# Kernel optimization log

Measured on AMD Instinct MI355X. Metric: run time of the kernel, lower is better.

Reference implementation:

```python
import jax, jax.numpy as jnp
import numpy as np

H = 1024      # hidden_dim
E = 512       # word_emb_dim
A = 512       # av_emb_dim
L = 512       # max_length
V = 50257     # n_vocab


def setup_inputs() -> dict:
    key = jax.random.key(0)
    ks = jax.random.split(key, 16)
    s = lambda k, shape, scale=0.02: (jax.random.normal(k, shape, dtype=jnp.float32) * scale)
    return {
        "word": jax.random.randint(ks[0], (1,), 0, V),
        "enc_seq_len": 1,
        "av_emb": s(ks[1], (1, A), 1.0),
        "h0": s(ks[2], (1, 1, H), 1.0),
        "c0": s(ks[3], (1, 1, H), 1.0),
        "encoder_outputs": s(ks[4], (L, H), 1.0),
        "emb_table": s(ks[5], (V, E)),
        "attn_W": s(ks[6], (L, E + H)),
        "attn_b": s(ks[7], (L,)),
        "comb_W": s(ks[8], (H, E + H + A)),
        "comb_b": s(ks[9], (H,)),
        "W_ih": s(ks[10], (4 * H, H)),
        "W_hh": s(ks[11], (4 * H, H)),
        "b_ih": s(ks[12], (4 * H,)),
        "b_hh": s(ks[13], (4 * H,)),
        "out_W": s(ks[14], (V, H)),
        "out_b": s(ks[15], (V,)),
    }


def reference(word, enc_seq_len, av_emb, h0, c0, encoder_outputs,
              emb_table, attn_W, attn_b, comb_W, comb_b,
              W_ih, W_hh, b_ih, b_hh, out_W, out_b):
    # embedded: [1, E]
    embedded = emb_table[word].reshape(1, -1)
    h = h0[0]  # [1, H]
    c = c0[0]  # [1, H]

    # attention scores over encoder positions: [1, L]
    attn_pre = jnp.concatenate([embedded, h], axis=1) @ attn_W.T + attn_b
    # faithful to original: rows >= enc_seq_len set to -inf (no-op for batch dim of 1 when enc_seq_len>=1)
    row = jnp.arange(attn_pre.shape[0])[:, None]
    attn_pre = jnp.where(row >= enc_seq_len, -jnp.inf, attn_pre)
    attn_weights = jax.nn.softmax(attn_pre, axis=1)           # [1, L]
    attn_applied = attn_weights @ encoder_outputs             # [1, H]

    # combine + relu: [1, H]
    comb = jnp.concatenate([embedded, attn_applied, av_emb], axis=1)
    x = jax.nn.relu(comb @ comb_W.T + comb_b)

    # single-step LSTM (torch gate order: i, f, g, o)
    gates = x @ W_ih.T + b_ih + h @ W_hh.T + b_hh             # [1, 4H]
    i, f, g, o = jnp.split(gates, 4, axis=1)
    c_new = jax.nn.sigmoid(f) * c + jax.nn.sigmoid(i) * jnp.tanh(g)
    h_new = jax.nn.sigmoid(o) * jnp.tanh(c_new)

    logits = h_new @ out_W.T + out_b                          # [1, V]
    return logits, h_new[None], c_new[None], attn_weights
```

## Files before the change

kernel.cpp:

```cpp
#include <hip/hip_runtime.h>


#define V 50257

#define WS_PRE    0
#define WS_ATTNW  512
#define WS_APPL   1024
#define WS_X      2048

#define OUT_H     50257
#define OUT_C     51281
#define OUT_AW    52305

__device__ __forceinline__ float4 ld4(const float* p) {
  return *reinterpret_cast<const float4*>(p);
}
__device__ __forceinline__ float dot4(float4 a, float4 b) {
  return a.x * b.x + a.y * b.y + a.z * b.z + a.w * b.w;
}
__device__ __forceinline__ float wave_reduce(float a) {
#pragma unroll
  for (int off = 32; off > 0; off >>= 1) a += __shfl_xor(a, off, 64);
  return a;
}
__device__ __forceinline__ float sigf(float v) {
  return 1.f / (1.f + expf(-v));
}

__global__ __launch_bounds__(256) void attn_mv_k(const float* __restrict__ attn_W,
                                                 const float* __restrict__ attn_b,
                                                 const float* __restrict__ emb,
                                                 const int* __restrict__ word,
                                                 const float* __restrict__ h0,
                                                 float* __restrict__ pre) {
  int row = blockIdx.x * 4 + (threadIdx.x >> 6);
  int lane = threadIdx.x & 63;
  const float* Wr = attn_W + (size_t)row * 1536;
  const float* er = emb + (size_t)word[0] * 512;
  float acc = 0.f;
#pragma unroll
  for (int k = 0; k < 2; k++) {
    int c = lane * 4 + k * 256;
    acc += dot4(ld4(Wr + c), ld4(er + c));
  }
#pragma unroll
  for (int k = 2; k < 6; k++) {
    int c = lane * 4 + k * 256;
    acc += dot4(ld4(Wr + c), ld4(h0 + c - 512));
  }
  acc = wave_reduce(acc);
  if (lane == 0) pre[row] = acc + attn_b[row];
}

__global__ __launch_bounds__(512) void softmax_k(const float* __restrict__ pre,
                                                 float* __restrict__ wout,
                                                 float* __restrict__ out_w,
                                                 float* __restrict__ applied) {
  __shared__ float red[8];
  __shared__ float stat[2];
  int t = threadIdx.x;
  int lane = t & 63, wid = t >> 6;
  applied[t] = 0.f;
  applied[512 + t] = 0.f;
  float v = pre[t];
  float m = v;
#pragma unroll
  for (int off = 32; off > 0; off >>= 1) m = fmaxf(m, __shfl_xor(m, off, 64));
  if (lane == 0) red[wid] = m;
  __syncthreads();
  if (t == 0) {
    float mm = red[0];
    for (int i = 1; i < 8; i++) mm = fmaxf(mm, red[i]);
    stat[0] = mm;
  }
  __syncthreads();
  float e = expf(v - stat[0]);
  float s = e;
#pragma unroll
  for (int off = 32; off > 0; off >>= 1) s += __shfl_xor(s, off, 64);
  if (lane == 0) red[wid] = s;
  __syncthreads();
  if (t == 0) {
    float ss = 0.f;
    for (int i = 0; i < 8; i++) ss += red[i];
    stat[1] = ss;
  }
  __syncthreads();
  float w = e / stat[1];
  wout[t] = w;
  out_w[t] = w;
}

__global__ __launch_bounds__(256) void attn_apply_k(const float* __restrict__ w,
                                                    const float* __restrict__ enc,
                                                    float* __restrict__ applied) {
  int jb = blockIdx.x & 3, lb = blockIdx.x >> 2;
  int j = jb * 256 + threadIdx.x;
  int l0 = lb * 64;
  float acc = 0.f;
#pragma unroll 4
  for (int l = l0; l < l0 + 64; l++) acc += w[l] * enc[(size_t)l * 1024 + j];
  atomicAdd(applied + j, acc);
}

__global__ __launch_bounds__(256) void comb_mv_k(const float* __restrict__ comb_W,
                                                 const float* __restrict__ comb_b,
                                                 const float* __restrict__ emb,
                                                 const int* __restrict__ word,
                                                 const float* __restrict__ applied,
                                                 const float* __restrict__ av,
                                                 float* __restrict__ x) {
  int row = blockIdx.x * 4 + (threadIdx.x >> 6);
  int lane = threadIdx.x & 63;
  const float* Wr = comb_W + (size_t)row * 2048;
  const float* er = emb + (size_t)word[0] * 512;
  float acc = 0.f;
#pragma unroll
  for (int k = 0; k < 2; k++) {
    int c = lane * 4 + k * 256;
    acc += dot4(ld4(Wr + c), ld4(er + c));
  }
#pragma unroll
  for (int k = 2; k < 6; k++) {
    int c = lane * 4 + k * 256;
    acc += dot4(ld4(Wr + c), ld4(applied + c - 512));
  }
#pragma unroll
  for (int k = 6; k < 8; k++) {
    int c = lane * 4 + k * 256;
    acc += dot4(ld4(Wr + c), ld4(av + c - 1536));
  }
  acc = wave_reduce(acc);
  if (lane == 0) x[row] = fmaxf(acc + comb_b[row], 0.f);
}

__global__ __launch_bounds__(256) void gates_lstm_k(const float* __restrict__ Wih,
                                                    const float* __restrict__ Whh,
                                                    const float* __restrict__ bih,
                                                    const float* __restrict__ bhh,
                                                    const float* __restrict__ x,
                                                    const float* __restrict__ h0,
                                                    const float* __restrict__ c0,
                                                    float* __restrict__ out_h,
                                                    float* __restrict__ out_c) {
  __shared__ float gsh[4];
  int t = blockIdx.x;
  int wv = threadIdx.x >> 6, lane = threadIdx.x & 63;
  size_t r = (size_t)wv * 1024 + t;
  const float* Wi = Wih + r * 1024;
  const float* Wh = Whh + r * 1024;
  float acc = 0.f;
#pragma unroll
  for (int k = 0; k < 4; k++) {
    int c = lane * 4 + k * 256;
    acc += dot4(ld4(Wi + c), ld4(x + c));
    acc += dot4(ld4(Wh + c), ld4(h0 + c));
  }
  acc = wave_reduce(acc);
  if (lane == 0) gsh[wv] = acc + bih[r] + bhh[r];
  __syncthreads();
  if (threadIdx.x == 0) {
    float gi = sigf(gsh[0]);
    float gf = sigf(gsh[1]);
    float gg = tanhf(gsh[2]);
    float go = sigf(gsh[3]);
    float cn = gf * c0[t] + gi * gg;
    float hn = go * tanhf(cn);
    out_h[t] = hn;
    out_c[t] = cn;
  }
}

__global__ __launch_bounds__(256) void logits_mv_k(const float* __restrict__ W,
                                                   const float* __restrict__ bias,
                                                   const float* __restrict__ x,
                                                   float* __restrict__ y) {
  int wv = threadIdx.x >> 6, lane = threadIdx.x & 63;
  int r0 = blockIdx.x * 8 + wv * 2;
  if (r0 >= V) return;
  bool has1 = (r0 + 1) < V;
  const float* W0 = W + (size_t)r0 * 1024;
  float a0 = 0.f, a1 = 0.f;
#pragma unroll
  for (int k = 0; k < 4; k++) {
    int c = lane * 4 + k * 256;
    float4 xv = ld4(x + c);
    a0 += dot4(ld4(W0 + c), xv);
    if (has1) a1 += dot4(ld4(W0 + 1024 + c), xv);
  }
  a0 = wave_reduce(a0);
  a1 = wave_reduce(a1);
  if (lane == 0) {
    y[r0] = a0 + bias[r0];
    if (has1) y[r0 + 1] = a1 + bias[r0 + 1];
  }
}

extern "C" void kernel_launch(void* const* d_in, const int* in_sizes, int n_in,
                              void* d_out, int out_size, void* d_ws, size_t ws_size,
                              hipStream_t stream) {
  const int*   word   = (const int*)  d_in[0];
  const float* av     = (const float*)d_in[2];
  const float* h0     = (const float*)d_in[3];
  const float* c0     = (const float*)d_in[4];
  const float* enc    = (const float*)d_in[5];
  const float* emb    = (const float*)d_in[6];
  const float* attn_W = (const float*)d_in[7];
  const float* attn_b = (const float*)d_in[8];
  const float* comb_W = (const float*)d_in[9];
  const float* comb_b = (const float*)d_in[10];
  const float* W_ih   = (const float*)d_in[11];
  const float* W_hh   = (const float*)d_in[12];
  const float* b_ih   = (const float*)d_in[13];
  const float* b_hh   = (const float*)d_in[14];
  const float* out_W  = (const float*)d_in[15];
  const float* out_b  = (const float*)d_in[16];

  float* ws  = (float*)d_ws;
  float* out = (float*)d_out;

  attn_mv_k<<<128, 256, 0, stream>>>(attn_W, attn_b, emb, word, h0, ws + WS_PRE);
  softmax_k<<<1, 512, 0, stream>>>(ws + WS_PRE, ws + WS_ATTNW, out + OUT_AW,
                                   ws + WS_APPL);
  attn_apply_k<<<32, 256, 0, stream>>>(ws + WS_ATTNW, enc, ws + WS_APPL);
  comb_mv_k<<<256, 256, 0, stream>>>(comb_W, comb_b, emb, word, ws + WS_APPL,
                                     av, ws + WS_X);
  gates_lstm_k<<<1024, 256, 0, stream>>>(W_ih, W_hh, b_ih, b_hh, ws + WS_X,
                                         h0, c0, out + OUT_H, out + OUT_C);
  logits_mv_k<<<(V + 7) / 8, 256, 0, stream>>>(out_W, out_b, out + OUT_H, out);
}
```

Baseline: 397.3 us.

## Fuse decoder step into one persistent kernel with grid barriers and out_W prefetch

Replaces the six dependent launches with a single 1024-block persistent kernel that separates stages with a software grid barrier. It hoists the W_hh·h0 product so it runs alongside the attention matvec. Blocks that sit idle in the small stages read slices of out_W to warm the cache before the logits matvec. The intent is to remove launch gaps and overlap the serial chain with the bandwidth-bound logits weight stream. The risks are that the grid barrier can deadlock if not all 1024 blocks are co-resident (it has a spin timeout, which would break correctness), and that the prefetched 16K rows may not stay resident in cache.

New measurement: 1.443 ms. +263.3%, slower.

```diff
diff --git a/kernel.cpp b/kernel.cpp
--- a/kernel.cpp
+++ b/kernel.cpp
@@ -1,12 +1,14 @@
 #include <hip/hip_runtime.h>
 
-
 #define V 50257
+#define NBLK 1024
 
 #define WS_PRE    0
 #define WS_ATTNW  512
 #define WS_APPL   1024
 #define WS_X      2048
+#define WS_GHH    3072
+#define WS_BAR    8192
 
 #define OUT_H     50257
 #define OUT_C     51281
@@ -27,172 +29,212 @@
   return 1.f / (1.f + expf(-v));
 }
 
-__global__ __launch_bounds__(256) void attn_mv_k(const float* __restrict__ attn_W,
-                                                 const float* __restrict__ attn_b,
-                                                 const float* __restrict__ emb,
-                                                 const int* __restrict__ word,
-                                                 const float* __restrict__ h0,
-                                                 float* __restrict__ pre) {
-  int row = blockIdx.x * 4 + (threadIdx.x >> 6);
-  int lane = threadIdx.x & 63;
-  const float* Wr = attn_W + (size_t)row * 1536;
-  const float* er = emb + (size_t)word[0] * 512;
-  float acc = 0.f;
-#pragma unroll
-  for (int k = 0; k < 2; k++) {
-    int c = lane * 4 + k * 256;
-    acc += dot4(ld4(Wr + c), ld4(er + c));
-  }
-#pragma unroll
-  for (int k = 2; k < 6; k++) {
-    int c = lane * 4 + k * 256;
-    acc += dot4(ld4(Wr + c), ld4(h0 + c - 512));
-  }
-  acc = wave_reduce(acc);
-  if (lane == 0) pre[row] = acc + attn_b[row];
-}
-
-__global__ __launch_bounds__(512) void softmax_k(const float* __restrict__ pre,
-                                                 float* __restrict__ wout,
-                                                 float* __restrict__ out_w,
-                                                 float* __restrict__ applied) {
-  __shared__ float red[8];
-  __shared__ float stat[2];
-  int t = threadIdx.x;
-  int lane = t & 63, wid = t >> 6;
-  applied[t] = 0.f;
-  applied[512 + t] = 0.f;
-  float v = pre[t];
-  float m = v;
-#pragma unroll
-  for (int off = 32; off > 0; off >>= 1) m = fmaxf(m, __shfl_xor(m, off, 64));
-  if (lane == 0) red[wid] = m;
-  __syncthreads();
-  if (t == 0) {
-    float mm = red[0];
-    for (int i = 1; i < 8; i++) mm = fmaxf(mm, red[i]);
-    stat[0] = mm;
-  }
-  __syncthreads();
-  float e = expf(v - stat[0]);
-  float s = e;
-#pragma unroll
-  for (int off = 32; off > 0; off >>= 1) s += __shfl_xor(s, off, 64);
-  if (lane == 0) red[wid] = s;
-  __syncthreads();
-  if (t == 0) {
-    float ss = 0.f;
-    for (int i = 0; i < 8; i++) ss += red[i];
-    stat[1] = ss;
-  }
-  __syncthreads();
-  float w = e / stat[1];
-  wout[t] = w;
-  out_w[t] = w;
-}
-
-__global__ __launch_bounds__(256) void attn_apply_k(const float* __restrict__ w,
-                                                    const float* __restrict__ enc,
-                                                    float* __restrict__ applied) {
-  int jb = blockIdx.x & 3, lb = blockIdx.x >> 2;
-  int j = jb * 256 + threadIdx.x;
-  int l0 = lb * 64;
-  float acc = 0.f;
-#pragma unroll 4
-  for (int l = l0; l < l0 + 64; l++) acc += w[l] * enc[(size_t)l * 1024 + j];
-  atomicAdd(applied + j, acc);
-}
-
-__global__ __launch_bounds__(256) void comb_mv_k(const float* __restrict__ comb_W,
-                                                 const float* __restrict__ comb_b,
-                                                 const float* __restrict__ emb,
-                                                 const int* __restrict__ word,
-                                                 const float* __restrict__ applied,
-                                                 const float* __restrict__ av,
-                                                 float* __restrict__ x) {
-  int row = blockIdx.x * 4 + (threadIdx.x >> 6);
-  int lane = threadIdx.x & 63;
-  const float* Wr = comb_W + (size_t)row * 2048;
-  const float* er = emb + (size_t)word[0] * 512;
-  float acc = 0.f;
-#pragma unroll
-  for (int k = 0; k < 2; k++) {
-    int c = lane * 4 + k * 256;
-    acc += dot4(ld4(Wr + c), ld4(er + c));
-  }
-#pragma unroll
-  for (int k = 2; k < 6; k++) {
-    int c = lane * 4 + k * 256;
-    acc += dot4(ld4(Wr + c), ld4(applied + c - 512));
-  }
-#pragma unroll
-  for (int k = 6; k < 8; k++) {
-    int c = lane * 4 + k * 256;
-    acc += dot4(ld4(Wr + c), ld4(av + c - 1536));
-  }
-  acc = wave_reduce(acc);
-  if (lane == 0) x[row] = fmaxf(acc + comb_b[row], 0.f);
-}
-
-__global__ __launch_bounds__(256) void gates_lstm_k(const float* __restrict__ Wih,
-                                                    const float* __restrict__ Whh,
-                                                    const float* __restrict__ bih,
-                                                    const float* __restrict__ bhh,
-                                                    const float* __restrict__ x,
-                                                    const float* __restrict__ h0,
-                                                    const float* __restrict__ c0,
-                                                    float* __restrict__ out_h,
-                                                    float* __restrict__ out_c) {
-  __shared__ float gsh[4];
-  int t = blockIdx.x;
-  int wv = threadIdx.x >> 6, lane = threadIdx.x & 63;
-  size_t r = (size_t)wv * 1024 + t;
-  const float* Wi = Wih + r * 1024;
-  const float* Wh = Whh + r * 1024;
-  float acc = 0.f;
-#pragma unroll
-  for (int k = 0; k < 4; k++) {
-    int c = lane * 4 + k * 256;
-    acc += dot4(ld4(Wi + c), ld4(x + c));
-    acc += dot4(ld4(Wh + c), ld4(h0 + c));
-  }
-  acc = wave_reduce(acc);
-  if (lane == 0) gsh[wv] = acc + bih[r] + bhh[r];
+__device__ __forceinline__ void grid_bar(int* bar) {
   __syncthreads();
   if (threadIdx.x == 0) {
-    float gi = sigf(gsh[0]);
-    float gf = sigf(gsh[1]);
-    float gg = tanhf(gsh[2]);
-    float go = sigf(gsh[3]);
-    float cn = gf * c0[t] + gi * gg;
-    float hn = go * tanhf(cn);
-    out_h[t] = hn;
-    out_c[t] = cn;
-  }
-}
-
-__global__ __launch_bounds__(256) void logits_mv_k(const float* __restrict__ W,
-                                                   const float* __restrict__ bias,
-                                                   const float* __restrict__ x,
-                                                   float* __restrict__ y) {
-  int wv = threadIdx.x >> 6, lane = threadIdx.x & 63;
-  int r0 = blockIdx.x * 8 + wv * 2;
-  if (r0 >= V) return;
-  bool has1 = (r0 + 1) < V;
-  const float* W0 = W + (size_t)r0 * 1024;
-  float a0 = 0.f, a1 = 0.f;
-#pragma unroll
-  for (int k = 0; k < 4; k++) {
-    int c = lane * 4 + k * 256;
-    float4 xv = ld4(x + c);
-    a0 += dot4(ld4(W0 + c), xv);
-    if (has1) a1 += dot4(ld4(W0 + 1024 + c), xv);
-  }
-  a0 = wave_reduce(a0);
-  a1 = wave_reduce(a1);
-  if (lane == 0) {
-    y[r0] = a0 + bias[r0];
-    if (has1) y[r0 + 1] = a1 + bias[r0 + 1];
+    __threadfence();
+    int g = __hip_atomic_load(bar + 1, __ATOMIC_RELAXED, __HIP_MEMORY_SCOPE_AGENT);
+    int a = __hip_atomic_fetch_add(bar, 1, __ATOMIC_ACQ_REL, __HIP_MEMORY_SCOPE_AGENT);
+    if (a == NBLK - 1) {
+      __hip_atomic_store(bar, 0, __ATOMIC_RELAXED, __HIP_MEMORY_SCOPE_AGENT);
+      __hip_atomic_store(bar + 1, g + 1, __ATOMIC_RELEASE, __HIP_MEMORY_SCOPE_AGENT);
+    } else {
+      long spin = 0;
+      while (__hip_atomic_load(bar + 1, __ATOMIC_ACQUIRE, __HIP_MEMORY_SCOPE_AGENT) == g) {
+        __builtin_amdgcn_s_sleep(2);
+        if (++spin > 4000000L) break;
+      }
+    }
+    __threadfence();
+  }
+  __syncthreads();
+}
+
+__device__ __forceinline__ void prefetch_rows(const float* __restrict__ W,
+                                              int row0, int nrows,
+                                              int bid, int nb, int t) {
+  const float4* p = reinterpret_cast<const float4*>(W) + (size_t)row0 * 256;
+  size_t n4 = (size_t)nrows * 256;
+  float sx = 0.f, sy = 0.f, sz = 0.f, sw = 0.f;
+  for (size_t i = (size_t)bid * 256 + t; i < n4; i += (size_t)nb * 256) {
+    float4 v = p[i];
+    sx += v.x; sy += v.y; sz += v.z; sw += v.w;
+  }
+  asm volatile("" :: "v"(sx), "v"(sy), "v"(sz), "v"(sw));
+}
+
+__global__ __launch_bounds__(256) void init_k(float* __restrict__ ws) {
+  int t = threadIdx.x;
+  if (t < 2) reinterpret_cast<int*>(ws + WS_BAR)[t] = 0;
+  for (int i = t; i < 1024; i += 256) ws[WS_APPL + i] = 0.f;
+}
+
+__global__ __launch_bounds__(256, 4) void fused_k(
+    const int* __restrict__ word, const float* __restrict__ av,
+    const float* __restrict__ h0, const float* __restrict__ c0,
+    const float* __restrict__ enc, const float* __restrict__ emb,
+    const float* __restrict__ attn_W, const float* __restrict__ attn_b,
+    const float* __restrict__ comb_W, const float* __restrict__ comb_b,
+    const float* __restrict__ W_ih, const float* __restrict__ W_hh,
+    const float* __restrict__ b_ih, const float* __restrict__ b_hh,
+    const float* __restrict__ out_W, const float* __restrict__ out_b,
+    float* __restrict__ ws, float* __restrict__ out) {
+  int* bar = reinterpret_cast<int*>(ws + WS_BAR);
+  const int b = blockIdx.x;
+  const int t = threadIdx.x;
+  const int wv = t >> 6, lane = t & 63;
+  const float* er = emb + (size_t)word[0] * 512;
+
+  if (b < 128) {
+    int row = b * 4 + wv;
+    const float* Wr = attn_W + (size_t)row * 1536;
+    float acc = 0.f;
+#pragma unroll
+    for (int k = 0; k < 2; k++) {
+      int c = lane * 4 + k * 256;
+      acc += dot4(ld4(Wr + c), ld4(er + c));
+    }
+#pragma unroll
+    for (int k = 2; k < 6; k++) {
+      int c = lane * 4 + k * 256;
+      acc += dot4(ld4(Wr + c), ld4(h0 + c - 512));
+    }
+    acc = wave_reduce(acc);
+    if (lane == 0) ws[WS_PRE + row] = acc + attn_b[row];
+  } else if (b < 256) {
+    int gid = (b - 128) * 4 + wv;
+#pragma unroll
+    for (int rr = 0; rr < 8; rr++) {
+      int r = gid * 8 + rr;
+      const float* Wh = W_hh + (size_t)r * 1024;
+      float acc = 0.f;
+#pragma unroll
+      for (int k = 0; k < 4; k++) {
+        int c = lane * 4 + k * 256;
+        acc += dot4(ld4(Wh + c), ld4(h0 + c));
+      }
+      acc = wave_reduce(acc);
+      if (lane == 0) ws[WS_GHH + r] = acc + b_hh[r];
+    }
+  } else {
+    prefetch_rows(out_W, 0, 6144, b - 256, 768, t);
+  }
+  grid_bar(bar);
+
+  if (b == 0) {
+    __shared__ float red[4];
+    __shared__ float stat[2];
+    float v0 = ws[WS_PRE + t], v1 = ws[WS_PRE + 256 + t];
+    float m = fmaxf(v0, v1);
+#pragma unroll
+    for (int off = 32; off > 0; off >>= 1) m = fmaxf(m, __shfl_xor(m, off, 64));
+    if (lane == 0) red[wv] = m;
+    __syncthreads();
+    if (t == 0) stat[0] = fmaxf(fmaxf(red[0], red[1]), fmaxf(red[2], red[3]));
+    __syncthreads();
+    float e0 = expf(v0 - stat[0]), e1 = expf(v1 - stat[0]);
+    float s = e0 + e1;
+#pragma unroll
+    for (int off = 32; off > 0; off >>= 1) s += __shfl_xor(s, off, 64);
+    if (lane == 0) red[wv] = s;
+    __syncthreads();
+    if (t == 0) stat[1] = red[0] + red[1] + red[2] + red[3];
+    __syncthreads();
+    float w0 = e0 / stat[1], w1 = e1 / stat[1];
+    ws[WS_ATTNW + t] = w0;
+    ws[WS_ATTNW + 256 + t] = w1;
+    out[OUT_AW + t] = w0;
+    out[OUT_AW + 256 + t] = w1;
+  } else {
+    prefetch_rows(out_W, 6144, 4096, b - 1, 1023, t);
+  }
+  grid_bar(bar);
+
+  if (b < 32) {
+    int jb = b & 3, lb = b >> 2;
+    int j = jb * 256 + t, l0 = lb * 64;
+    float acc = 0.f;
+#pragma unroll 4
+    for (int l = l0; l < l0 + 64; l++)
+      acc += ws[WS_ATTNW + l] * enc[(size_t)l * 1024 + j];
+    atomicAdd(ws + WS_APPL + j, acc);
+  } else {
+    prefetch_rows(out_W, 10240, 4096, b - 32, 992, t);
+  }
+  grid_bar(bar);
+
+  if (b < 256) {
+    int row = b * 4 + wv;
+    const float* Wr = comb_W + (size_t)row * 2048;
+    float acc = 0.f;
+#pragma unroll
+    for (int k = 0; k < 2; k++) {
+      int c = lane * 4 + k * 256;
+      acc += dot4(ld4(Wr + c), ld4(er + c));
+    }
+#pragma unroll
+    for (int k = 2; k < 6; k++) {
+      int c = lane * 4 + k * 256;
+      acc += dot4(ld4(Wr + c), ld4(ws + WS_APPL + c - 512));
+    }
+#pragma unroll
+    for (int k = 6; k < 8; k++) {
+      int c = lane * 4 + k * 256;
+      acc += dot4(ld4(Wr + c), ld4(av + c - 1536));
+    }
+    acc = wave_reduce(acc);
+    if (lane == 0) ws[WS_X + row] = fmaxf(acc + comb_b[row], 0.f);
+  } else {
+    prefetch_rows(out_W, 14336, 4096, b - 256, 768, t);
+  }
+  grid_bar(bar);
+
+  {
+    __shared__ float gsh[4];
+    size_t r = (size_t)wv * 1024 + b;
+    const float* Wi = W_ih + r * 1024;
+    float acc = 0.f;
+#pragma unroll
+    for (int k = 0; k < 4; k++) {
+      int c = lane * 4 + k * 256;
+      acc += dot4(ld4(Wi + c), ld4(ws + WS_X + c));
+    }
+    acc = wave_reduce(acc);
+    if (lane == 0) gsh[wv] = acc + b_ih[r] + ws[WS_GHH + r];
+    __syncthreads();
+    if (t == 0) {
+      float gi = sigf(gsh[0]);
+      float gf = sigf(gsh[1]);
+      float gg = tanhf(gsh[2]);
+      float go = sigf(gsh[3]);
+      float cn = gf * c0[b] + gi * gg;
+      float hn = go * tanhf(cn);
+      out[OUT_H + b] = hn;
+      out[OUT_C + b] = cn;
+    }
+  }
+  grid_bar(bar);
+
+  const float* hx = out + OUT_H;
+  for (int g = b; g < 6283; g += NBLK) {
+    int r0 = g * 8 + wv * 2;
+    if (r0 >= V) continue;
+    bool has1 = (r0 + 1) < V;
+    const float* W0 = out_W + (size_t)r0 * 1024;
+    float a0 = 0.f, a1 = 0.f;
+#pragma unroll
+    for (int k = 0; k < 4; k++) {
+      int c = lane * 4 + k * 256;
+      float4 xv = ld4(hx + c);
+      a0 += dot4(ld4(W0 + c), xv);
+      if (has1) a1 += dot4(ld4(W0 + 1024 + c), xv);
+    }
+    a0 = wave_reduce(a0);
+    a1 = wave_reduce(a1);
+    if (lane == 0) {
+      out[r0] = a0 + out_b[r0];
+      if (has1) out[r0 + 1] = a1 + out_b[r0 + 1];
+    }
   }
 }
 
@@ -219,13 +261,8 @@
   float* ws  = (float*)d_ws;
   float* out = (float*)d_out;
 
-  attn_mv_k<<<128, 256, 0, stream>>>(attn_W, attn_b, emb, word, h0, ws + WS_PRE);
-  softmax_k<<<1, 512, 0, stream>>>(ws + WS_PRE, ws + WS_ATTNW, out + OUT_AW,
-                                   ws + WS_APPL);
-  attn_apply_k<<<32, 256, 0, stream>>>(ws + WS_ATTNW, enc, ws + WS_APPL);
-  comb_mv_k<<<256, 256, 0, stream>>>(comb_W, comb_b, emb, word, ws + WS_APPL,
-                                     av, ws + WS_X);
-  gates_lstm_k<<<1024, 256, 0, stream>>>(W_ih, W_hh, b_ih, b_hh, ws + WS_X,
-                                         h0, c0, out + OUT_H, out + OUT_C);
-  logits_mv_k<<<(V + 7) / 8, 256, 0, stream>>>(out_W, out_b, out + OUT_H, out);
-}
+  init_k<<<1, 256, 0, stream>>>(ws);
+  fused_k<<<NBLK, 256, 0, stream>>>(word, av, h0, c0, enc, emb, attn_W, attn_b,
+                                    comb_W, comb_b, W_ih, W_hh, b_ih, b_hh,
+                                    out_W, out_b, ws, out);
+}
```

## Hoist W_hh gate matvec into first kernel and fuse softmax with attention apply

Applied to the files above, without the earlier changes.

Moves the h0·W_hh gate product, which only depends on inputs, into the first kernel alongside the attention score matvec, so the 16MB W_hh read happens early instead of inside the LSTM gate kernel. Fuses the softmax into the attention-apply kernel, with every block recomputing the 512-element softmax and the enc reduction split across 64 blocks, which removes one launch and the workspace round trip. This cuts the kernel count from six to five. The cost is redundant softmax work per block and a first kernel with imbalanced branches, since the W_hh blocks do eight rows per wave.

Result: no change. 394.9 us (-0.6%).

```diff
diff --git a/kernel.cpp b/kernel.cpp
--- a/kernel.cpp
+++ b/kernel.cpp
@@ -1,12 +1,11 @@
 #include <hip/hip_runtime.h>
 
-
 #define V 50257
 
 #define WS_PRE    0
-#define WS_ATTNW  512
 #define WS_APPL   1024
 #define WS_X      2048
+#define WS_GHH    3072
 
 #define OUT_H     50257
 #define OUT_C     51281
@@ -27,89 +26,94 @@
   return 1.f / (1.f + expf(-v));
 }
 
-__global__ __launch_bounds__(256) void attn_mv_k(const float* __restrict__ attn_W,
-                                                 const float* __restrict__ attn_b,
-                                                 const float* __restrict__ emb,
-                                                 const int* __restrict__ word,
-                                                 const float* __restrict__ h0,
-                                                 float* __restrict__ pre) {
-  int row = blockIdx.x * 4 + (threadIdx.x >> 6);
-  int lane = threadIdx.x & 63;
-  const float* Wr = attn_W + (size_t)row * 1536;
-  const float* er = emb + (size_t)word[0] * 512;
+__global__ __launch_bounds__(256) void pre_ghh_k(
+    const float* __restrict__ attn_W, const float* __restrict__ attn_b,
+    const float* __restrict__ emb, const int* __restrict__ word,
+    const float* __restrict__ h0, const float* __restrict__ W_hh,
+    const float* __restrict__ b_hh, float* __restrict__ ws) {
+  int b = blockIdx.x;
+  int t = threadIdx.x, wv = t >> 6, lane = t & 63;
+  if (b < 128) {
+    int row = b * 4 + wv;
+    const float* Wr = attn_W + (size_t)row * 1536;
+    const float* er = emb + (size_t)word[0] * 512;
+    float acc = 0.f;
+#pragma unroll
+    for (int k = 0; k < 2; k++) {
+      int c = lane * 4 + k * 256;
+      acc += dot4(ld4(Wr + c), ld4(er + c));
+    }
+#pragma unroll
+    for (int k = 2; k < 6; k++) {
+      int c = lane * 4 + k * 256;
+      acc += dot4(ld4(Wr + c), ld4(h0 + c - 512));
+    }
+    acc = wave_reduce(acc);
+    if (lane == 0) ws[WS_PRE + row] = acc + attn_b[row];
+  } else if (b < 256) {
+    int gid = (b - 128) * 4 + wv;
+#pragma unroll
+    for (int rr = 0; rr < 8; rr++) {
+      int r = gid * 8 + rr;
+      const float* Wh = W_hh + (size_t)r * 1024;
+      float acc = 0.f;
+#pragma unroll
+      for (int k = 0; k < 4; k++) {
+        int c = lane * 4 + k * 256;
+        acc += dot4(ld4(Wh + c), ld4(h0 + c));
+      }
+      acc = wave_reduce(acc);
+      if (lane == 0) ws[WS_GHH + r] = acc + b_hh[r];
+    }
+  } else {
+    for (int i = t; i < 1024; i += 256) ws[WS_APPL + i] = 0.f;
+  }
+}
+
+__global__ __launch_bounds__(256) void sm_apply_k(
+    const float* __restrict__ pre, const float* __restrict__ enc,
+    float* __restrict__ out_w, float* __restrict__ applied) {
+  __shared__ float wsh[512];
+  __shared__ float red[4];
+  __shared__ float stat[2];
+  int t = threadIdx.x, lane = t & 63, wv = t >> 6;
+  float v0 = pre[t], v1 = pre[t + 256];
+  float m = fmaxf(v0, v1);
+#pragma unroll
+  for (int off = 32; off > 0; off >>= 1) m = fmaxf(m, __shfl_xor(m, off, 64));
+  if (lane == 0) red[wv] = m;
+  __syncthreads();
+  if (t == 0) stat[0] = fmaxf(fmaxf(red[0], red[1]), fmaxf(red[2], red[3]));
+  __syncthreads();
+  float e0 = expf(v0 - stat[0]), e1 = expf(v1 - stat[0]);
+  float s = e0 + e1;
+#pragma unroll
+  for (int off = 32; off > 0; off >>= 1) s += __shfl_xor(s, off, 64);
+  if (lane == 0) red[wv] = s;
+  __syncthreads();
+  if (t == 0) stat[1] = red[0] + red[1] + red[2] + red[3];
+  __syncthreads();
+  float w0 = e0 / stat[1], w1 = e1 / stat[1];
+  wsh[t] = w0;
+  wsh[t + 256] = w1;
+  if (blockIdx.x == 0) {
+    out_w[t] = w0;
+    out_w[t + 256] = w1;
+  }
+  __syncthreads();
+  int jb = blockIdx.x & 3, lb = blockIdx.x >> 2;
+  int j = jb * 256 + t, l0 = lb * 32;
   float acc = 0.f;
-#pragma unroll
-  for (int k = 0; k < 2; k++) {
-    int c = lane * 4 + k * 256;
-    acc += dot4(ld4(Wr + c), ld4(er + c));
-  }
-#pragma unroll
-  for (int k = 2; k < 6; k++) {
-    int c = lane * 4 + k * 256;
-    acc += dot4(ld4(Wr + c), ld4(h0 + c - 512));
-  }
-  acc = wave_reduce(acc);
-  if (lane == 0) pre[row] = acc + attn_b[row];
-}
-
-__global__ __launch_bounds__(512) void softmax_k(const float* __restrict__ pre,
-                                                 float* __restrict__ wout,
-                                                 float* __restrict__ out_w,
-                                                 float* __restrict__ applied) {
-  __shared__ float red[8];
-  __shared__ float stat[2];
-  int t = threadIdx.x;
-  int lane = t & 63, wid = t >> 6;
-  applied[t] = 0.f;
-  applied[512 + t] = 0.f;
-  float v = pre[t];
-  float m = v;
-#pragma unroll
-  for (int off = 32; off > 0; off >>= 1) m = fmaxf(m, __shfl_xor(m, off, 64));
-  if (lane == 0) red[wid] = m;
-  __syncthreads();
-  if (t == 0) {
-    float mm = red[0];
-    for (int i = 1; i < 8; i++) mm = fmaxf(mm, red[i]);
-    stat[0] = mm;
-  }
-  __syncthreads();
-  float e = expf(v - stat[0]);
-  float s = e;
-#pragma unroll
-  for (int off = 32; off > 0; off >>= 1) s += __shfl_xor(s, off, 64);
-  if (lane == 0) red[wid] = s;
-  __syncthreads();
-  if (t == 0) {
-    float ss = 0.f;
-    for (int i = 0; i < 8; i++) ss += red[i];
-    stat[1] = ss;
-  }
-  __syncthreads();
-  float w = e / stat[1];
-  wout[t] = w;
-  out_w[t] = w;
-}
-
-__global__ __launch_bounds__(256) void attn_apply_k(const float* __restrict__ w,
-                                                    const float* __restrict__ enc,
-                                                    float* __restrict__ applied) {
-  int jb = blockIdx.x & 3, lb = blockIdx.x >> 2;
-  int j = jb * 256 + threadIdx.x;
-  int l0 = lb * 64;
-  float acc = 0.f;
-#pragma unroll 4
-  for (int l = l0; l < l0 + 64; l++) acc += w[l] * enc[(size_t)l * 1024 + j];
+#pragma unroll 8
+  for (int l = l0; l < l0 + 32; l++) acc += wsh[l] * enc[(size_t)l * 1024 + j];
   atomicAdd(applied + j, acc);
 }
 
-__global__ __launch_bounds__(256) void comb_mv_k(const float* __restrict__ comb_W,
-                                                 const float* __restrict__ comb_b,
-                                                 const float* __restrict__ emb,
-                                                 const int* __restrict__ word,
-                                                 const float* __restrict__ applied,
-                                                 const float* __restrict__ av,
-                                                 float* __restrict__ x) {
+__global__ __launch_bounds__(256) void comb_mv_k(
+    const float* __restrict__ comb_W, const float* __restrict__ comb_b,
+    const float* __restrict__ emb, const int* __restrict__ word,
+    const float* __restrict__ applied, const float* __restrict__ av,
+    float* __restrict__ x) {
   int row = blockIdx.x * 4 + (threadIdx.x >> 6);
   int lane = threadIdx.x & 63;
   const float* Wr = comb_W + (size_t)row * 2048;
@@ -134,30 +138,24 @@
   if (lane == 0) x[row] = fmaxf(acc + comb_b[row], 0.f);
 }
 
-__global__ __launch_bounds__(256) void gates_lstm_k(const float* __restrict__ Wih,
-                                                    const float* __restrict__ Whh,
-                                                    const float* __restrict__ bih,
-                                                    const float* __restrict__ bhh,
-                                                    const float* __restrict__ x,
-                                                    const float* __restrict__ h0,
-                                                    const float* __restrict__ c0,
-                                                    float* __restrict__ out_h,
-                                                    float* __restrict__ out_c) {
+__global__ __launch_bounds__(256) void gates_lstm_k(
+    const float* __restrict__ Wih, const float* __restrict__ bih,
+    const float* __restrict__ ghh, const float* __restrict__ x,
+    const float* __restrict__ c0, float* __restrict__ out_h,
+    float* __restrict__ out_c) {
   __shared__ float gsh[4];
   int t = blockIdx.x;
   int wv = threadIdx.x >> 6, lane = threadIdx.x & 63;
   size_t r = (size_t)wv * 1024 + t;
   const float* Wi = Wih + r * 1024;
-  const float* Wh = Whh + r * 1024;
   float acc = 0.f;
 #pragma unroll
   for (int k = 0; k < 4; k++) {
     int c = lane * 4 + k * 256;
     acc += dot4(ld4(Wi + c), ld4(x + c));
-    acc += dot4(ld4(Wh + c), ld4(h0 + c));
   }
   acc = wave_reduce(acc);
-  if (lane == 0) gsh[wv] = acc + bih[r] + bhh[r];
+  if (lane == 0) gsh[wv] = acc + bih[r] + ghh[r];
   __syncthreads();
   if (threadIdx.x == 0) {
     float gi = sigf(gsh[0]);
@@ -171,10 +169,9 @@
   }
 }
 
-__global__ __launch_bounds__(256) void logits_mv_k(const float* __restrict__ W,
-                                                   const float* __restrict__ bias,
-                                                   const float* __restrict__ x,
-                                                   float* __restrict__ y) {
+__global__ __launch_bounds__(256) void logits_mv_k(
+    const float* __restrict__ W, const float* __restrict__ bias,
+    const float* __restrict__ x, float* __restrict__ y) {
   int wv = threadIdx.x >> 6, lane = threadIdx.x & 63;
   int r0 = blockIdx.x * 8 + wv * 2;
   if (r0 >= V) return;
@@ -219,13 +216,13 @@
   float* ws  = (float*)d_ws;
   float* out = (float*)d_out;
 
-  attn_mv_k<<<128, 256, 0, stream>>>(attn_W, attn_b, emb, word, h0, ws + WS_PRE);
-  softmax_k<<<1, 512, 0, stream>>>(ws + WS_PRE, ws + WS_ATTNW, out + OUT_AW,
-                                   ws + WS_APPL);
-  attn_apply_k<<<32, 256, 0, stream>>>(ws + WS_ATTNW, enc, ws + WS_APPL);
+  pre_ghh_k<<<257, 256, 0, stream>>>(attn_W, attn_b, emb, word, h0, W_hh,
+                                     b_hh, ws);
+  sm_apply_k<<<64, 256, 0, stream>>>(ws + WS_PRE, enc, out + OUT_AW,
+                                     ws + WS_APPL);
   comb_mv_k<<<256, 256, 0, stream>>>(comb_W, comb_b, emb, word, ws + WS_APPL,
                                      av, ws + WS_X);
-  gates_lstm_k<<<1024, 256, 0, stream>>>(W_ih, W_hh, b_ih, b_hh, ws + WS_X,
-                                         h0, c0, out + OUT_H, out + OUT_C);
+  gates_lstm_k<<<1024, 256, 0, stream>>>(W_ih, b_ih, ws + WS_GHH, ws + WS_X,
+                                         c0, out + OUT_H, out + OUT_C);
   logits_mv_k<<<(V + 7) / 8, 256, 0, stream>>>(out_W, out_b, out + OUT_H, out);
 }
```
